# Performance work log

Measured on AMD Instinct MI355X. Metric: run time of the kernel, lower is better.

Reference implementation:

```python
import jax, jax.numpy as jnp
import numpy as np

TQ, TK, B, D = 2, 5, 16384, 512

def setup_inputs() -> dict:
    key = jax.random.key(0)
    ks = jax.random.split(key, 6)
    s = 1.0 / np.sqrt(D)
    return {
        "h": jax.random.normal(ks[0], (TQ, B, D), dtype=jnp.float32),
        "enc_out": jax.random.normal(ks[1], (TK, B, D), dtype=jnp.float32),
        "Wq": jax.random.normal(ks[2], (D, D), dtype=jnp.float32) * s,
        "Wk": jax.random.normal(ks[3], (D, D), dtype=jnp.float32) * s,
        "Wv": jax.random.normal(ks[4], (D, D), dtype=jnp.float32) * s,
        "Wdown": jax.random.normal(ks[5], (2 * D, D), dtype=jnp.float32) * (1.0 / np.sqrt(2 * D)),
    }

def reference(h, enc_out, Wq, Wk, Wv, Wdown):
    # h: [Tq, B, D] -> [B, Tq, D]; enc_out: [Tk, B, D] -> [B, Tk, D]
    hb = jnp.transpose(h, (1, 0, 2))
    eb = jnp.transpose(enc_out, (1, 0, 2))
    q = hb @ Wq            # [B, Tq, D]
    k = eb @ Wk            # [B, Tk, D]
    v = eb @ Wv            # [B, Tk, D]
    qk = jnp.einsum('bij,bkj->bik', q, k)       # [B, Tq, Tk]
    att = jax.nn.softmax(qk, axis=-1)
    att_out = jnp.einsum('bij,bjk->bik', att, v) # [B, Tq, D]
    cat = jnp.concatenate([hb, att_out], axis=2) # [B, Tq, 2D]
    out = cat @ Wdown                            # [B, Tq, D]
    return jnp.transpose(out, (1, 0, 2))         # [Tq, B, D]
```

## Files before the change

kernel.cpp:

```cpp
#include <hip/hip_runtime.h>
#include <hip/hip_fp16.h>


#define B_TOT   16384
#define TQn     2
#define TKn     5
#define NB      32
#define ROWS    64
#define THREADS 1024
#define WCOLS   32

typedef _Float16 f16;
typedef _Float16 f16x8 __attribute__((ext_vector_type(8)));
typedef _Float16 f16x4 __attribute__((ext_vector_type(4)));
typedef float    f32x4 __attribute__((ext_vector_type(4)));

#define HPAN 0
#define TPAN 65536
#define LDS_TOTAL 131072

#define MFMA16(a, b, c) __builtin_amdgcn_mfma_f32_16x16x32_f16(a, b, c, 0, 0, 0)

__global__ __launch_bounds__(THREADS, 4) void fused_attn(
    const float* __restrict__ hptr, const float* __restrict__ eptr,
    const f16* __restrict__ Mt, const f16* __restrict__ Wdt,
    float* __restrict__ outp)
{
  extern __shared__ char smem[];
  const int tid  = threadIdx.x;
  const int lane = tid & 63;
  const int w    = tid >> 6;
  const int g    = lane >> 4;
  const int l15  = lane & 15;
  const int b0   = blockIdx.x * NB;
  const int n0   = w * WCOLS;
  const int xsw  = (l15 & 7) << 4;

  #pragma unroll
  for (int i = 0; i < 8; ++i) {
    int c   = tid + THREADS * i;
    int row = c >> 7;
    int k4  = c & 127;
    int tq  = row & 1;
    int b   = b0 + (row >> 1);
    float4 v = *reinterpret_cast<const float4*>(
        hptr + ((size_t)(tq * B_TOT + b) << 9) + (k4 << 2));
    f16x4 p;
    p[0] = (f16)v.x; p[1] = (f16)v.y; p[2] = (f16)v.z; p[3] = (f16)v.w;
    *reinterpret_cast<f16x4*>(smem + HPAN + row * 1024 +
                              (((k4 << 3)) ^ ((row & 7) << 4))) = p;
  }

  const f16* bpM = Mt + (size_t)(n0 + l15) * 512 + (g << 3);
  f16x8 bc0 = *reinterpret_cast<const f16x8*>(bpM);
  f16x8 bc1 = *reinterpret_cast<const f16x8*>(bpM + 16 * 512);

  __syncthreads();

  f32x4 accT[4][2];
  #pragma unroll
  for (int fm = 0; fm < 4; ++fm) {
    accT[fm][0] = (f32x4){0.f, 0.f, 0.f, 0.f};
    accT[fm][1] = (f32x4){0.f, 0.f, 0.f, 0.f};
  }
  for (int kt = 0; kt < 16; ++kt) {
    f16x8 af[4];
    #pragma unroll
    for (int fm = 0; fm < 4; ++fm) {
      int row = (fm << 4) + l15;
      af[fm] = *reinterpret_cast<const f16x8*>(
          smem + HPAN + row * 1024 + (((kt << 6) + (g << 4)) ^ xsw));
    }
    if (kt < 15) {
      f16x8 bn0 = *reinterpret_cast<const f16x8*>(bpM + (kt + 1) * 32);
      f16x8 bn1 = *reinterpret_cast<const f16x8*>(bpM + 16 * 512 + (kt + 1) * 32);
      #pragma unroll
      for (int fm = 0; fm < 4; ++fm) {
        accT[fm][0] = MFMA16(af[fm], bc0, accT[fm][0]);
        accT[fm][1] = MFMA16(af[fm], bc1, accT[fm][1]);
      }
      bc0 = bn0; bc1 = bn1;
    } else {
      #pragma unroll
      for (int fm = 0; fm < 4; ++fm) {
        accT[fm][0] = MFMA16(af[fm], bc0, accT[fm][0]);
        accT[fm][1] = MFMA16(af[fm], bc1, accT[fm][1]);
      }
    }
  }

  #pragma unroll
  for (int fm = 0; fm < 4; ++fm)
    #pragma unroll
    for (int fn = 0; fn < 2; ++fn)
      #pragma unroll
      for (int r = 0; r < 4; ++r) {
        int row = (fm << 4) + (g << 2) + r;
        int col = n0 + (fn << 4) + l15;
        *reinterpret_cast<f16*>(smem + TPAN + row * 1024 +
                                (((col << 1)) ^ ((row & 7) << 4))) = (f16)accT[fm][fn][r];
      }
  __syncthreads();

  for (int bi = 0; bi < 2; ++bi) {
    const int bl = (w << 1) + bi;
    const int b  = b0 + bl;
    float ev[TKn][8];
    #pragma unroll
    for (int j = 0; j < TKn; ++j) {
      const float4* p4 = reinterpret_cast<const float4*>(
          eptr + ((size_t)(j * B_TOT + b) << 9) + (lane << 3));
      float4 u0 = p4[0], u1 = p4[1];
      ev[j][0] = u0.x; ev[j][1] = u0.y; ev[j][2] = u0.z; ev[j][3] = u0.w;
      ev[j][4] = u1.x; ev[j][5] = u1.y; ev[j][6] = u1.z; ev[j][7] = u1.w;
    }
    float tv[TQn][8];
    #pragma unroll
    for (int i = 0; i < TQn; ++i) {
      int row = (bl << 1) + i;
      f16x8 tf = *reinterpret_cast<const f16x8*>(
          smem + TPAN + row * 1024 + (((lane << 4)) ^ ((row & 7) << 4)));
      #pragma unroll
      for (int m = 0; m < 8; ++m) tv[i][m] = (float)tf[m];
    }
    float p[TQn][TKn];
    #pragma unroll
    for (int i = 0; i < TQn; ++i)
      #pragma unroll
      for (int j = 0; j < TKn; ++j) {
        float s = 0.f;
        #pragma unroll
        for (int m = 0; m < 8; ++m) s += tv[i][m] * ev[j][m];
        p[i][j] = s;
      }
    #pragma unroll
    for (int d = 1; d < 64; d <<= 1)
      #pragma unroll
      for (int i = 0; i < TQn; ++i)
        #pragma unroll
        for (int j = 0; j < TKn; ++j)
          p[i][j] += __shfl_xor(p[i][j], d, 64);
    #pragma unroll
    for (int i = 0; i < TQn; ++i) {
      float mx = p[i][0];
      #pragma unroll
      for (int j = 1; j < TKn; ++j) mx = fmaxf(mx, p[i][j]);
      float sum = 0.f;
      #pragma unroll
      for (int j = 0; j < TKn; ++j) { float e = __expf(p[i][j] - mx); p[i][j] = e; sum += e; }
      float rs = 1.0f / sum;
      int row = (bl << 1) + i;
      f16x8 uv;
      #pragma unroll
      for (int m = 0; m < 8; ++m) {
        float s = 0.f;
        #pragma unroll
        for (int j = 0; j < TKn; ++j) s += p[i][j] * ev[j][m];
        uv[m] = (f16)(s * rs);
      }
      *reinterpret_cast<f16x8*>(
          smem + TPAN + row * 1024 + (((lane << 4)) ^ ((row & 7) << 4))) = uv;
    }
  }
  __syncthreads();

  const f16* bpW = Wdt + (size_t)(n0 + l15) * 1024 + (g << 3);
  bc0 = *reinterpret_cast<const f16x8*>(bpW);
  bc1 = *reinterpret_cast<const f16x8*>(bpW + 16 * 1024);
  f32x4 accP[4][2];
  #pragma unroll
  for (int fm = 0; fm < 4; ++fm) {
    accP[fm][0] = (f32x4){0.f, 0.f, 0.f, 0.f};
    accP[fm][1] = (f32x4){0.f, 0.f, 0.f, 0.f};
  }
  for (int kt = 0; kt < 32; ++kt) {
    char* ab = smem + ((kt >> 4) << 16);
    f16x8 af[4];
    #pragma unroll
    for (int fm = 0; fm < 4; ++fm) {
      int row = (fm << 4) + l15;
      af[fm] = *reinterpret_cast<const f16x8*>(
          ab + row * 1024 + ((((kt & 15) << 6) + (g << 4)) ^ xsw));
    }
    if (kt < 31) {
      f16x8 bn0 = *reinterpret_cast<const f16x8*>(bpW + (kt + 1) * 32);
      f16x8 bn1 = *reinterpret_cast<const f16x8*>(bpW + 16 * 1024 + (kt + 1) * 32);
      #pragma unroll
      for (int fm = 0; fm < 4; ++fm) {
        accP[fm][0] = MFMA16(af[fm], bc0, accP[fm][0]);
        accP[fm][1] = MFMA16(af[fm], bc1, accP[fm][1]);
      }
      bc0 = bn0; bc1 = bn1;
    } else {
      #pragma unroll
      for (int fm = 0; fm < 4; ++fm) {
        accP[fm][0] = MFMA16(af[fm], bc0, accP[fm][0]);
        accP[fm][1] = MFMA16(af[fm], bc1, accP[fm][1]);
      }
    }
  }

  #pragma unroll
  for (int fm = 0; fm < 4; ++fm)
    #pragma unroll
    for (int fn = 0; fn < 2; ++fn)
      #pragma unroll
      for (int r = 0; r < 4; ++r) {
        int row = (fm << 4) + (g << 2) + r;
        int col = n0 + (fn << 4) + l15;
        int tq  = row & 1;
        int b   = b0 + (row >> 1);
        outp[((size_t)(tq * B_TOT + b) << 9) + col] = accP[fm][fn][r];
      }
}

__global__ __launch_bounds__(256) void prep_all(
    const float* __restrict__ Wq, const float* __restrict__ Wk,
    const float* __restrict__ Wv, const float* __restrict__ Wdown,
    f16* __restrict__ Mt, f16* __restrict__ Wdt)
{
  __shared__ float sA[32][68];
  __shared__ float sB[32][68];
  const int tid = threadIdx.x;
  const int bx  = blockIdx.x;

  if (bx < 512) {
    const bool mt  = (bx < 256);
    const int  bb  = mt ? bx : bx - 256;
    const int  n0  = (bb & 15) << 5;
    const int  k0  = (bb >> 4) << 5;
    float accv[4] = {0.f, 0.f, 0.f, 0.f};
    for (int e0 = 0; e0 < 512; e0 += 64) {
      if (mt) {
        #pragma unroll
        for (int i = 0; i < 2; ++i) {
          int c = tid + (i << 8);
          int r = c >> 4, e4 = (c & 15) << 2;
          *reinterpret_cast<float4*>(&sA[r][e4]) =
              *reinterpret_cast<const float4*>(Wq + ((k0 + r) << 9) + e0 + e4);
          *reinterpret_cast<float4*>(&sB[r][e4]) =
              *reinterpret_cast<const float4*>(Wk + ((n0 + r) << 9) + e0 + e4);
        }
      } else {
        #pragma unroll
        for (int i = 0; i < 2; ++i) {
          int c = tid + (i << 8);
          int r = c >> 4, e4 = (c & 15) << 2;
          *reinterpret_cast<float4*>(&sA[r][e4]) =
              *reinterpret_cast<const float4*>(Wv + ((k0 + r) << 9) + e0 + e4);
        }
        #pragma unroll
        for (int i = 0; i < 8; ++i) {
          int c = tid + (i << 8);
          int el = c >> 5, nl = c & 31;
          sB[nl][el] = Wdown[((512 + e0 + el) << 9) + n0 + nl];
        }
      }
      __syncthreads();
      #pragma unroll
      for (int i = 0; i < 4; ++i) {
        int o = tid + (i << 8);
        int nl = o >> 5, kl = o & 31;
        float s = accv[i];
        #pragma unroll
        for (int e = 0; e < 64; e += 4) {
          float4 a  = *reinterpret_cast<const float4*>(&sA[kl][e]);
          float4 bq = *reinterpret_cast<const float4*>(&sB[nl][e]);
          s += a.x * bq.x + a.y * bq.y + a.z * bq.z + a.w * bq.w;
        }
        accv[i] = s;
      }
      __syncthreads();
    }
    #pragma unroll
    for (int i = 0; i < 4; ++i) {
      int o = tid + (i << 8);
      int nl = o >> 5, kl = o & 31;
      if (mt) Mt[((n0 + nl) << 9) + k0 + kl] = (f16)accv[i];
      else    Wdt[((n0 + nl) << 10) + 512 + k0 + kl] = (f16)accv[i];
    }
  } else {
    const int bb = bx - 512;
    const int n0 = (bb & 15) << 5;
    const int k0 = (bb >> 4) << 5;
    #pragma unroll
    for (int i = 0; i < 4; ++i) {
      int c = tid + (i << 8);
      int r = c >> 5, nl = c & 31;
      sA[r][nl] = Wdown[((k0 + r) << 9) + n0 + nl];
    }
    __syncthreads();
    #pragma unroll
    for (int i = 0; i < 4; ++i) {
      int c = tid + (i << 8);
      int nl = c >> 5, kl = c & 31;
      Wdt[((n0 + nl) << 10) + k0 + kl] = (f16)sA[kl][nl];
    }
  }
}

extern "C" void kernel_launch(void* const* d_in, const int* in_sizes, int n_in,
                              void* d_out, int out_size, void* d_ws, size_t ws_size,
                              hipStream_t stream) {
  const float* h   = (const float*)d_in[0];
  const float* enc = (const float*)d_in[1];
  const float* Wq  = (const float*)d_in[2];
  const float* Wk  = (const float*)d_in[3];
  const float* Wv  = (const float*)d_in[4];
  const float* Wd  = (const float*)d_in[5];
  float* out = (float*)d_out;

  f16* Mt  = (f16*)d_ws;
  f16* Wdt = Mt + 512 * 512;

  (void)hipFuncSetAttribute(reinterpret_cast<const void*>(fused_attn),
                            hipFuncAttributeMaxDynamicSharedMemorySize, LDS_TOTAL);

  prep_all<<<768, 256, 0, stream>>>(Wq, Wk, Wv, Wd, Mt, Wdt);
  fused_attn<<<B_TOT / NB, THREADS, LDS_TOTAL, stream>>>(h, enc, Mt, Wdt, out);
}
```

Baseline: 189.7 us.

## Halve batch tile per block, prefetch encoder rows early, use fdot2 scores

After: 290.9 us. +53.3%, slower.

```diff
diff --git a/kernel.cpp b/kernel.cpp
--- a/kernel.cpp
+++ b/kernel.cpp
@@ -5,23 +5,23 @@
 #define B_TOT   16384
 #define TQn     2
 #define TKn     5
-#define NB      32
-#define ROWS    64
+#define NB      16
+#define ROWS    32
 #define THREADS 1024
-#define WCOLS   32
 
 typedef _Float16 f16;
 typedef _Float16 f16x8 __attribute__((ext_vector_type(8)));
 typedef _Float16 f16x4 __attribute__((ext_vector_type(4)));
+typedef _Float16 f16x2 __attribute__((ext_vector_type(2)));
 typedef float    f32x4 __attribute__((ext_vector_type(4)));
 
 #define HPAN 0
-#define TPAN 65536
-#define LDS_TOTAL 131072
+#define TPAN 32768
+#define LDS_TOTAL 65536
 
 #define MFMA16(a, b, c) __builtin_amdgcn_mfma_f32_16x16x32_f16(a, b, c, 0, 0, 0)
 
-__global__ __launch_bounds__(THREADS, 4) void fused_attn(
+__global__ __launch_bounds__(THREADS, 8) void fused_attn(
     const float* __restrict__ hptr, const float* __restrict__ eptr,
     const f16* __restrict__ Mt, const f16* __restrict__ Wdt,
     float* __restrict__ outp)
@@ -33,11 +33,11 @@
   const int g    = lane >> 4;
   const int l15  = lane & 15;
   const int b0   = blockIdx.x * NB;
-  const int n0   = w * WCOLS;
+  const int n0   = w * 32;
   const int xsw  = (l15 & 7) << 4;
 
   #pragma unroll
-  for (int i = 0; i < 8; ++i) {
+  for (int i = 0; i < 4; ++i) {
     int c   = tid + THREADS * i;
     int row = c >> 7;
     int k4  = c & 127;
@@ -48,7 +48,7 @@
     f16x4 p;
     p[0] = (f16)v.x; p[1] = (f16)v.y; p[2] = (f16)v.z; p[3] = (f16)v.w;
     *reinterpret_cast<f16x4*>(smem + HPAN + row * 1024 +
-                              (((k4 << 3)) ^ ((row & 7) << 4))) = p;
+                              ((k4 << 3) ^ ((row & 7) << 4))) = p;
   }
 
   const f16* bpM = Mt + (size_t)(n0 + l15) * 512 + (g << 3);
@@ -57,40 +57,43 @@
 
   __syncthreads();
 
-  f32x4 accT[4][2];
-  #pragma unroll
-  for (int fm = 0; fm < 4; ++fm) {
-    accT[fm][0] = (f32x4){0.f, 0.f, 0.f, 0.f};
-    accT[fm][1] = (f32x4){0.f, 0.f, 0.f, 0.f};
-  }
+  f32x4 acc[2][2];
+  #pragma unroll
+  for (int fm = 0; fm < 2; ++fm)
+    #pragma unroll
+    for (int fn = 0; fn < 2; ++fn)
+      acc[fm][fn] = (f32x4){0.f, 0.f, 0.f, 0.f};
   for (int kt = 0; kt < 16; ++kt) {
-    f16x8 af[4];
-    #pragma unroll
-    for (int fm = 0; fm < 4; ++fm) {
-      int row = (fm << 4) + l15;
-      af[fm] = *reinterpret_cast<const f16x8*>(
-          smem + HPAN + row * 1024 + (((kt << 6) + (g << 4)) ^ xsw));
-    }
+    f16x8 af0 = *reinterpret_cast<const f16x8*>(
+        smem + HPAN + l15 * 1024 + (((kt << 6) + (g << 4)) ^ xsw));
+    f16x8 af1 = *reinterpret_cast<const f16x8*>(
+        smem + HPAN + (16 + l15) * 1024 + (((kt << 6) + (g << 4)) ^ xsw));
+    f16x8 bn0, bn1;
     if (kt < 15) {
-      f16x8 bn0 = *reinterpret_cast<const f16x8*>(bpM + (kt + 1) * 32);
-      f16x8 bn1 = *reinterpret_cast<const f16x8*>(bpM + 16 * 512 + (kt + 1) * 32);
-      #pragma unroll
-      for (int fm = 0; fm < 4; ++fm) {
-        accT[fm][0] = MFMA16(af[fm], bc0, accT[fm][0]);
-        accT[fm][1] = MFMA16(af[fm], bc1, accT[fm][1]);
-      }
-      bc0 = bn0; bc1 = bn1;
-    } else {
-      #pragma unroll
-      for (int fm = 0; fm < 4; ++fm) {
-        accT[fm][0] = MFMA16(af[fm], bc0, accT[fm][0]);
-        accT[fm][1] = MFMA16(af[fm], bc1, accT[fm][1]);
-      }
-    }
-  }
-
-  #pragma unroll
-  for (int fm = 0; fm < 4; ++fm)
+      bn0 = *reinterpret_cast<const f16x8*>(bpM + (kt + 1) * 32);
+      bn1 = *reinterpret_cast<const f16x8*>(bpM + 16 * 512 + (kt + 1) * 32);
+    }
+    __builtin_amdgcn_s_setprio(1);
+    acc[0][0] = MFMA16(af0, bc0, acc[0][0]);
+    acc[0][1] = MFMA16(af0, bc1, acc[0][1]);
+    acc[1][0] = MFMA16(af1, bc0, acc[1][0]);
+    acc[1][1] = MFMA16(af1, bc1, acc[1][1]);
+    __builtin_amdgcn_s_setprio(0);
+    if (kt < 15) { bc0 = bn0; bc1 = bn1; }
+  }
+
+  const int b = b0 + w;
+  float4 e0[TKn], e1[TKn];
+  #pragma unroll
+  for (int j = 0; j < TKn; ++j) {
+    const float4* p4 = reinterpret_cast<const float4*>(
+        eptr + ((size_t)(j * B_TOT + b) << 9) + (lane << 3));
+    e0[j] = p4[0];
+    e1[j] = p4[1];
+  }
+
+  #pragma unroll
+  for (int fm = 0; fm < 2; ++fm)
     #pragma unroll
     for (int fn = 0; fn < 2; ++fn)
       #pragma unroll
@@ -98,110 +101,101 @@
         int row = (fm << 4) + (g << 2) + r;
         int col = n0 + (fn << 4) + l15;
         *reinterpret_cast<f16*>(smem + TPAN + row * 1024 +
-                                (((col << 1)) ^ ((row & 7) << 4))) = (f16)accT[fm][fn][r];
+                                ((col << 1) ^ ((row & 7) << 4))) = (f16)acc[fm][fn][r];
       }
   __syncthreads();
 
-  for (int bi = 0; bi < 2; ++bi) {
-    const int bl = (w << 1) + bi;
-    const int b  = b0 + bl;
-    float ev[TKn][8];
+  f16x8 evh[TKn];
+  #pragma unroll
+  for (int j = 0; j < TKn; ++j) {
+    evh[j][0] = (f16)e0[j].x; evh[j][1] = (f16)e0[j].y;
+    evh[j][2] = (f16)e0[j].z; evh[j][3] = (f16)e0[j].w;
+    evh[j][4] = (f16)e1[j].x; evh[j][5] = (f16)e1[j].y;
+    evh[j][6] = (f16)e1[j].z; evh[j][7] = (f16)e1[j].w;
+  }
+  f16x8 tvh[TQn];
+  #pragma unroll
+  for (int i = 0; i < TQn; ++i) {
+    int row = (w << 1) + i;
+    tvh[i] = *reinterpret_cast<const f16x8*>(
+        smem + TPAN + row * 1024 + ((lane << 4) ^ ((row & 7) << 4)));
+  }
+  float s[TQn][TKn];
+  #pragma unroll
+  for (int i = 0; i < TQn; ++i)
     #pragma unroll
     for (int j = 0; j < TKn; ++j) {
-      const float4* p4 = reinterpret_cast<const float4*>(
-          eptr + ((size_t)(j * B_TOT + b) << 9) + (lane << 3));
-      float4 u0 = p4[0], u1 = p4[1];
-      ev[j][0] = u0.x; ev[j][1] = u0.y; ev[j][2] = u0.z; ev[j][3] = u0.w;
-      ev[j][4] = u1.x; ev[j][5] = u1.y; ev[j][6] = u1.z; ev[j][7] = u1.w;
-    }
-    float tv[TQn][8];
-    #pragma unroll
-    for (int i = 0; i < TQn; ++i) {
-      int row = (bl << 1) + i;
-      f16x8 tf = *reinterpret_cast<const f16x8*>(
-          smem + TPAN + row * 1024 + (((lane << 4)) ^ ((row & 7) << 4)));
-      #pragma unroll
-      for (int m = 0; m < 8; ++m) tv[i][m] = (float)tf[m];
-    }
-    float p[TQn][TKn];
+      float acc_s = 0.f;
+      #pragma unroll
+      for (int p = 0; p < 4; ++p) {
+        f16x2 ta = {tvh[i][2 * p], tvh[i][2 * p + 1]};
+        f16x2 ea = {evh[j][2 * p], evh[j][2 * p + 1]};
+        acc_s = __builtin_amdgcn_fdot2(ta, ea, acc_s, false);
+      }
+      s[i][j] = acc_s;
+    }
+  #pragma unroll
+  for (int d = 1; d < 64; d <<= 1)
     #pragma unroll
     for (int i = 0; i < TQn; ++i)
       #pragma unroll
-      for (int j = 0; j < TKn; ++j) {
-        float s = 0.f;
-        #pragma unroll
-        for (int m = 0; m < 8; ++m) s += tv[i][m] * ev[j][m];
-        p[i][j] = s;
-      }
-    #pragma unroll
-    for (int d = 1; d < 64; d <<= 1)
-      #pragma unroll
-      for (int i = 0; i < TQn; ++i)
-        #pragma unroll
-        for (int j = 0; j < TKn; ++j)
-          p[i][j] += __shfl_xor(p[i][j], d, 64);
-    #pragma unroll
-    for (int i = 0; i < TQn; ++i) {
-      float mx = p[i][0];
-      #pragma unroll
-      for (int j = 1; j < TKn; ++j) mx = fmaxf(mx, p[i][j]);
-      float sum = 0.f;
-      #pragma unroll
-      for (int j = 0; j < TKn; ++j) { float e = __expf(p[i][j] - mx); p[i][j] = e; sum += e; }
-      float rs = 1.0f / sum;
-      int row = (bl << 1) + i;
-      f16x8 uv;
-      #pragma unroll
-      for (int m = 0; m < 8; ++m) {
-        float s = 0.f;
-        #pragma unroll
-        for (int j = 0; j < TKn; ++j) s += p[i][j] * ev[j][m];
-        uv[m] = (f16)(s * rs);
-      }
-      *reinterpret_cast<f16x8*>(
-          smem + TPAN + row * 1024 + (((lane << 4)) ^ ((row & 7) << 4))) = uv;
-    }
-  }
-  __syncthreads();
+      for (int j = 0; j < TKn; ++j)
+        s[i][j] += __shfl_xor(s[i][j], d, 64);
+  #pragma unroll
+  for (int i = 0; i < TQn; ++i) {
+    float mx = s[i][0];
+    #pragma unroll
+    for (int j = 1; j < TKn; ++j) mx = fmaxf(mx, s[i][j]);
+    float sum = 0.f;
+    #pragma unroll
+    for (int j = 0; j < TKn; ++j) { float e = __expf(s[i][j] - mx); s[i][j] = e; sum += e; }
+    float rs = 1.0f / sum;
+    int row = (w << 1) + i;
+    f16x8 uv;
+    #pragma unroll
+    for (int m = 0; m < 8; ++m) {
+      float uacc = 0.f;
+      #pragma unroll
+      for (int j = 0; j < TKn; ++j) uacc += s[i][j] * (float)evh[j][m];
+      uv[m] = (f16)(uacc * rs);
+    }
+    *reinterpret_cast<f16x8*>(
+        smem + TPAN + row * 1024 + ((lane << 4) ^ ((row & 7) << 4))) = uv;
+  }
 
   const f16* bpW = Wdt + (size_t)(n0 + l15) * 1024 + (g << 3);
   bc0 = *reinterpret_cast<const f16x8*>(bpW);
   bc1 = *reinterpret_cast<const f16x8*>(bpW + 16 * 1024);
-  f32x4 accP[4][2];
-  #pragma unroll
-  for (int fm = 0; fm < 4; ++fm) {
-    accP[fm][0] = (f32x4){0.f, 0.f, 0.f, 0.f};
-    accP[fm][1] = (f32x4){0.f, 0.f, 0.f, 0.f};
-  }
+  __syncthreads();
+
+  f32x4 acc2[2][2];
+  #pragma unroll
+  for (int fm = 0; fm < 2; ++fm)
+    #pragma unroll
+    for (int fn = 0; fn < 2; ++fn)
+      acc2[fm][fn] = (f32x4){0.f, 0.f, 0.f, 0.f};
   for (int kt = 0; kt < 32; ++kt) {
-    char* ab = smem + ((kt >> 4) << 16);
-    f16x8 af[4];
-    #pragma unroll
-    for (int fm = 0; fm < 4; ++fm) {
-      int row = (fm << 4) + l15;
-      af[fm] = *reinterpret_cast<const f16x8*>(
-          ab + row * 1024 + ((((kt & 15) << 6) + (g << 4)) ^ xsw));
-    }
+    char* ab = smem + ((kt >> 4) << 15);
+    f16x8 af0 = *reinterpret_cast<const f16x8*>(
+        ab + l15 * 1024 + ((((kt & 15) << 6) + (g << 4)) ^ xsw));
+    f16x8 af1 = *reinterpret_cast<const f16x8*>(
+        ab + (16 + l15) * 1024 + ((((kt & 15) << 6) + (g << 4)) ^ xsw));
+    f16x8 bn0, bn1;
     if (kt < 31) {
-      f16x8 bn0 = *reinterpret_cast<const f16x8*>(bpW + (kt + 1) * 32);
-      f16x8 bn1 = *reinterpret_cast<const f16x8*>(bpW + 16 * 1024 + (kt + 1) * 32);
-      #pragma unroll
-      for (int fm = 0; fm < 4; ++fm) {
-        accP[fm][0] = MFMA16(af[fm], bc0, accP[fm][0]);
-        accP[fm][1] = MFMA16(af[fm], bc1, accP[fm][1]);
-      }
-      bc0 = bn0; bc1 = bn1;
-    } else {
-      #pragma unroll
-      for (int fm = 0; fm < 4; ++fm) {
-        accP[fm][0] = MFMA16(af[fm], bc0, accP[fm][0]);
-        accP[fm][1] = MFMA16(af[fm], bc1, accP[fm][1]);
-      }
-    }
-  }
-
-  #pragma unroll
-  for (int fm = 0; fm < 4; ++fm)
+      bn0 = *reinterpret_cast<const f16x8*>(bpW + (kt + 1) * 32);
+      bn1 = *reinterpret_cast<const f16x8*>(bpW + 16 * 1024 + (kt + 1) * 32);
+    }
+    __builtin_amdgcn_s_setprio(1);
+    acc2[0][0] = MFMA16(af0, bc0, acc2[0][0]);
+    acc2[0][1] = MFMA16(af0, bc1, acc2[0][1]);
+    acc2[1][0] = MFMA16(af1, bc0, acc2[1][0]);
+    acc2[1][1] = MFMA16(af1, bc1, acc2[1][1]);
+    __builtin_amdgcn_s_setprio(0);
+    if (kt < 31) { bc0 = bn0; bc1 = bn1; }
+  }
+
+  #pragma unroll
+  for (int fm = 0; fm < 2; ++fm)
     #pragma unroll
     for (int fn = 0; fn < 2; ++fn)
       #pragma unroll
@@ -209,8 +203,8 @@
         int row = (fm << 4) + (g << 2) + r;
         int col = n0 + (fn << 4) + l15;
         int tq  = row & 1;
-        int b   = b0 + (row >> 1);
-        outp[((size_t)(tq * B_TOT + b) << 9) + col] = accP[fm][fn][r];
+        int bb  = b0 + (row >> 1);
+        outp[((size_t)(tq * B_TOT + bb) << 9) + col] = acc2[fm][fn][r];
       }
 }
 
@@ -261,14 +255,14 @@
       for (int i = 0; i < 4; ++i) {
         int o = tid + (i << 8);
         int nl = o >> 5, kl = o & 31;
-        float s = accv[i];
+        float sacc = accv[i];
         #pragma unroll
         for (int e = 0; e < 64; e += 4) {
           float4 a  = *reinterpret_cast<const float4*>(&sA[kl][e]);
           float4 bq = *reinterpret_cast<const float4*>(&sB[nl][e]);
-          s += a.x * bq.x + a.y * bq.y + a.z * bq.z + a.w * bq.w;
+          sacc += a.x * bq.x + a.y * bq.y + a.z * bq.z + a.w * bq.w;
         }
-        accv[i] = s;
+        accv[i] = sacc;
       }
       __syncthreads();
     }
```
